# Kernel optimization log

Hardware: AMD Instinct MI355X
Metric: run time of the kernel (lower is better)

Reference implementation:

```python
import jax, jax.numpy as jnp
import numpy as np

NUM_GRAPHS = 1024
IN_F = 256
HID = 512


def setup_inputs() -> dict:
    key = jax.random.key(0)
    ks = jax.random.split(key, 20)
    s_in = 1.0 / np.sqrt(IN_F)
    s_h = 1.0 / np.sqrt(HID)
    inp = {
        "x": jax.random.normal(ks[0], (200000, IN_F), dtype=jnp.float32),
        "batch": jnp.sort(jax.random.randint(ks[1], (200000,), 0, NUM_GRAPHS)),
        # transforms: Linear(in_features -> hidden)
        "W_mean": jax.random.uniform(ks[2], (IN_F, HID), jnp.float32, -s_in, s_in),
        "b_mean": jax.random.uniform(ks[3], (HID,), jnp.float32, -s_in, s_in),
        "W_max": jax.random.uniform(ks[4], (IN_F, HID), jnp.float32, -s_in, s_in),
        "b_max": jax.random.uniform(ks[5], (HID,), jnp.float32, -s_in, s_in),
        "W_sum": jax.random.uniform(ks[6], (IN_F, HID), jnp.float32, -s_in, s_in),
        "b_sum": jax.random.uniform(ks[7], (HID,), jnp.float32, -s_in, s_in),
        # gates: Linear(hidden -> 1) + sigmoid
        "g_mean_w": jax.random.uniform(ks[8], (HID, 1), jnp.float32, -s_h, s_h),
        "g_mean_b": jax.random.uniform(ks[9], (1,), jnp.float32, -s_h, s_h),
        "g_max_w": jax.random.uniform(ks[10], (HID, 1), jnp.float32, -s_h, s_h),
        "g_max_b": jax.random.uniform(ks[11], (1,), jnp.float32, -s_h, s_h),
        "g_sum_w": jax.random.uniform(ks[12], (HID, 1), jnp.float32, -s_h, s_h),
        "g_sum_b": jax.random.uniform(ks[13], (1,), jnp.float32, -s_h, s_h),
        # output proj: Linear(hidden -> in_features)
        "W_out": jax.random.uniform(ks[14], (HID, IN_F), jnp.float32, -s_h, s_h),
        "b_out": jax.random.uniform(ks[15], (IN_F,), jnp.float32, -s_h, s_h),
        # layer norm params
        "ln_gamma": jnp.ones((IN_F,), jnp.float32),
        "ln_beta": jnp.zeros((IN_F,), jnp.float32),
    }
    return inp


def reference(x, batch, W_mean, b_mean, W_max, b_max, W_sum, b_sum,
              g_mean_w, g_mean_b, g_max_w, g_max_b, g_sum_w, g_sum_b,
              W_out, b_out, ln_gamma, ln_beta):
    # --- segment pools over node dim ---
    sum_pool = jax.ops.segment_sum(x, batch, num_segments=NUM_GRAPHS)  # [G, F]
    counts = jax.ops.segment_sum(jnp.ones((x.shape[0],), x.dtype), batch,
                                 num_segments=NUM_GRAPHS)  # [G]
    mean_pool = sum_pool / jnp.maximum(counts, 1.0)[:, None]
    max_pool = jax.ops.segment_max(x, batch, num_segments=NUM_GRAPHS)
    max_pool = jnp.where(counts[:, None] > 0, max_pool, 0.0)

    # --- per-pool linear transforms ---
    mean_repr = mean_pool @ W_mean + b_mean  # [G, H]
    max_repr = max_pool @ W_max + b_max
    sum_repr = sum_pool @ W_sum + b_sum

    # --- gated fusion ---
    g_mean = jax.nn.sigmoid(mean_repr @ g_mean_w + g_mean_b)  # [G, 1]
    g_max = jax.nn.sigmoid(max_repr @ g_max_w + g_max_b)
    g_sum = jax.nn.sigmoid(sum_repr @ g_sum_w + g_sum_b)
    gates = jax.nn.softmax(jnp.concatenate([g_mean, g_max, g_sum], axis=1), axis=1)
    pooled = (gates[:, 0:1] * mean_repr + gates[:, 1:2] * max_repr
              + gates[:, 2:3] * sum_repr)

    # --- output projection (+dropout as eval identity) + layer norm ---
    emb = pooled @ W_out + b_out  # [G, F]
    mu = jnp.mean(emb, axis=-1, keepdims=True)
    var = jnp.var(emb, axis=-1, keepdims=True)
    emb = (emb - mu) * jax.lax.rsqrt(var + 1e-5) * ln_gamma + ln_beta
    return emb
```

## Files before the change

kernel.cpp:

```cpp
#include <hip/hip_runtime.h>
#include <math.h>

#define NUM_GRAPHS 1024
#define IN_F 256
#define HID 512

__device__ __forceinline__ int lower_bound_i(const int* __restrict__ b, int n, int v) {
    int lo = 0, hi = n;
    while (lo < hi) {
        int mid = (lo + hi) >> 1;
        if (b[mid] < v) lo = mid + 1; else hi = mid;
    }
    return lo;
}

__global__ __launch_bounds__(256) void pool_kernel(
    const float* __restrict__ x, const int* __restrict__ batch, int N,
    float* __restrict__ sum_pool, float* __restrict__ mean_pool,
    float* __restrict__ max_pool)
{
    int g = blockIdx.x;
    __shared__ int sb[2];
    if (threadIdx.x < 2) sb[threadIdx.x] = lower_bound_i(batch, N, g + (int)threadIdx.x);
    __syncthreads();
    int start = sb[0], end = sb[1];
    int f = threadIdx.x;
    const float* xp = x + f;
    float s = 0.f;
    float mx = -INFINITY;
    int r = start;
    for (; r + 8 <= end; r += 8) {
        float v0 = xp[(size_t)(r+0)*IN_F];
        float v1 = xp[(size_t)(r+1)*IN_F];
        float v2 = xp[(size_t)(r+2)*IN_F];
        float v3 = xp[(size_t)(r+3)*IN_F];
        float v4 = xp[(size_t)(r+4)*IN_F];
        float v5 = xp[(size_t)(r+5)*IN_F];
        float v6 = xp[(size_t)(r+6)*IN_F];
        float v7 = xp[(size_t)(r+7)*IN_F];
        s += ((v0+v1)+(v2+v3)) + ((v4+v5)+(v6+v7));
        mx = fmaxf(mx, fmaxf(fmaxf(fmaxf(v0,v1), fmaxf(v2,v3)),
                             fmaxf(fmaxf(v4,v5), fmaxf(v6,v7))));
    }
    for (; r < end; ++r) {
        float v = xp[(size_t)r*IN_F];
        s += v; mx = fmaxf(mx, v);
    }
    int cnt = end - start;
    float mean = s / fmaxf((float)cnt, 1.0f);
    if (cnt == 0) mx = 0.f;
    int o = g*IN_F + f;
    sum_pool[o]  = s;
    mean_pool[o] = mean;
    max_pool[o]  = mx;
}

#define BM 64
#define BN 32
#define BKK 32
__global__ __launch_bounds__(256) void transform_gemm(
    const float* __restrict__ p_mean, const float* __restrict__ p_max, const float* __restrict__ p_sum,
    const float* __restrict__ Wm, const float* __restrict__ bm_,
    const float* __restrict__ Wx, const float* __restrict__ bx_,
    const float* __restrict__ Wsm, const float* __restrict__ bs_,
    float* __restrict__ r_mean, float* __restrict__ r_max, float* __restrict__ r_sum)
{
    int z = blockIdx.z;
    const float* P    = (z==0) ? p_mean : (z==1) ? p_max : p_sum;
    const float* W    = (z==0) ? Wm     : (z==1) ? Wx    : Wsm;
    const float* bias = (z==0) ? bm_    : (z==1) ? bx_   : bs_;
    float* R          = (z==0) ? r_mean : (z==1) ? r_max : r_sum;

    __shared__ float As[BKK][BM+1];
    __shared__ float Bs[BKK][BN+1];
    int tid = threadIdx.x;
    int bm0 = blockIdx.y * BM;
    int bn0 = blockIdx.x * BN;
    int ty = tid >> 4, tx = tid & 15;
    int m0 = ty * 4, n0 = tx * 2;
    float acc[4][2] = {};

    for (int kc = 0; kc < IN_F; kc += BKK) {
        #pragma unroll
        for (int i = 0; i < 8; ++i) {
            int idx = tid + i*256;
            int rr = idx >> 5, cc = idx & 31;
            As[cc][rr] = P[(bm0 + rr)*IN_F + kc + cc];
        }
        #pragma unroll
        for (int i = 0; i < 4; ++i) {
            int idx = tid + i*256;
            int rr = idx >> 5, cc = idx & 31;
            Bs[rr][cc] = W[(kc + rr)*HID + bn0 + cc];
        }
        __syncthreads();
        #pragma unroll
        for (int k = 0; k < BKK; ++k) {
            float a0 = As[k][m0+0], a1 = As[k][m0+1];
            float a2 = As[k][m0+2], a3 = As[k][m0+3];
            float b0 = Bs[k][n0+0], b1 = Bs[k][n0+1];
            acc[0][0] += a0*b0; acc[0][1] += a0*b1;
            acc[1][0] += a1*b0; acc[1][1] += a1*b1;
            acc[2][0] += a2*b0; acc[2][1] += a2*b1;
            acc[3][0] += a3*b0; acc[3][1] += a3*b1;
        }
        __syncthreads();
    }
    #pragma unroll
    for (int i = 0; i < 4; ++i) {
        #pragma unroll
        for (int j = 0; j < 2; ++j) {
            int row = bm0 + m0 + i, col = bn0 + n0 + j;
            R[(size_t)row*HID + col] = acc[i][j] + bias[col];
        }
    }
}

__global__ __launch_bounds__(256) void gate_fuse(
    const float* __restrict__ r_mean, const float* __restrict__ r_max, const float* __restrict__ r_sum,
    const float* __restrict__ gwm, const float* __restrict__ gbm,
    const float* __restrict__ gwx, const float* __restrict__ gbx,
    const float* __restrict__ gws, const float* __restrict__ gbs,
    float* __restrict__ pooled)
{
    int g = blockIdx.x;
    int tid = threadIdx.x;
    size_t base = (size_t)g * HID;
    int h0 = tid, h1 = tid + 256;
    float m0 = r_mean[base+h0], m1 = r_mean[base+h1];
    float x0 = r_max[base+h0],  x1 = r_max[base+h1];
    float s0 = r_sum[base+h0],  s1 = r_sum[base+h1];
    float pm = m0*gwm[h0] + m1*gwm[h1];
    float px = x0*gwx[h0] + x1*gwx[h1];
    float ps = s0*gws[h0] + s1*gws[h1];
    #pragma unroll
    for (int off = 32; off > 0; off >>= 1) {
        pm += __shfl_xor(pm, off, 64);
        px += __shfl_xor(px, off, 64);
        ps += __shfl_xor(ps, off, 64);
    }
    __shared__ float red[3][4];
    __shared__ float wgt[3];
    int wv = tid >> 6, lane = tid & 63;
    if (lane == 0) { red[0][wv] = pm; red[1][wv] = px; red[2][wv] = ps; }
    __syncthreads();
    if (tid == 0) {
        float dm  = red[0][0]+red[0][1]+red[0][2]+red[0][3] + gbm[0];
        float dx  = red[1][0]+red[1][1]+red[1][2]+red[1][3] + gbx[0];
        float dsv = red[2][0]+red[2][1]+red[2][2]+red[2][3] + gbs[0];
        float sm = 1.f/(1.f+expf(-dm));
        float sx = 1.f/(1.f+expf(-dx));
        float ss = 1.f/(1.f+expf(-dsv));
        float em = expf(sm), ex = expf(sx), es = expf(ss);
        float inv = 1.f/(em+ex+es);
        wgt[0] = em*inv; wgt[1] = ex*inv; wgt[2] = es*inv;
    }
    __syncthreads();
    float wm = wgt[0], wxx = wgt[1], wss = wgt[2];
    pooled[base+h0] = wm*m0 + wxx*x0 + wss*s0;
    pooled[base+h1] = wm*m1 + wxx*x1 + wss*s1;
}

#define EM 4
__global__ __launch_bounds__(256) void outproj_ln(
    const float* __restrict__ pooled, const float* __restrict__ Wout, const float* __restrict__ bout,
    const float* __restrict__ gamma, const float* __restrict__ beta, float* __restrict__ out)
{
    int gbase = blockIdx.x * EM;
    int tid = threadIdx.x;
    __shared__ float Ps[EM][HID];
    __shared__ float Es[EM][IN_F];
    const float4* pp = (const float4*)(pooled + (size_t)gbase * HID);
    float4* ps4 = (float4*)&Ps[0][0];
    ps4[tid]       = pp[tid];
    ps4[tid + 256] = pp[tid + 256];
    __syncthreads();
    float acc0=0.f, acc1=0.f, acc2=0.f, acc3=0.f;
    int f = tid;
    #pragma unroll 4
    for (int k = 0; k < HID; ++k) {
        float w = Wout[(size_t)k*IN_F + f];
        acc0 += Ps[0][k]*w;
        acc1 += Ps[1][k]*w;
        acc2 += Ps[2][k]*w;
        acc3 += Ps[3][k]*w;
    }
    float bo = bout[f];
    Es[0][f] = acc0+bo; Es[1][f] = acc1+bo; Es[2][f] = acc2+bo; Es[3][f] = acc3+bo;
    __syncthreads();
    int w = tid >> 6;
    int lane = tid & 63;
    float v0 = Es[w][lane], v1 = Es[w][lane+64], v2 = Es[w][lane+128], v3 = Es[w][lane+192];
    float s  = v0+v1+v2+v3;
    float sq = v0*v0+v1*v1+v2*v2+v3*v3;
    #pragma unroll
    for (int off = 32; off > 0; off >>= 1) {
        s  += __shfl_xor(s, off, 64);
        sq += __shfl_xor(sq, off, 64);
    }
    float mu  = s * (1.0f/IN_F);
    float var = sq * (1.0f/IN_F) - mu*mu;
    float rs  = rsqrtf(var + 1e-5f);
    float* orow = out + (size_t)(gbase + w) * IN_F;
    orow[lane]     = (v0-mu)*rs*gamma[lane]     + beta[lane];
    orow[lane+64]  = (v1-mu)*rs*gamma[lane+64]  + beta[lane+64];
    orow[lane+128] = (v2-mu)*rs*gamma[lane+128] + beta[lane+128];
    orow[lane+192] = (v3-mu)*rs*gamma[lane+192] + beta[lane+192];
}

extern "C" void kernel_launch(void* const* d_in, const int* in_sizes, int n_in,
                              void* d_out, int out_size, void* d_ws, size_t ws_size,
                              hipStream_t stream)
{
    const float* x        = (const float*)d_in[0];
    const int*   batch    = (const int*)d_in[1];
    const float* W_mean   = (const float*)d_in[2];
    const float* b_mean   = (const float*)d_in[3];
    const float* W_max    = (const float*)d_in[4];
    const float* b_max    = (const float*)d_in[5];
    const float* W_sum    = (const float*)d_in[6];
    const float* b_sum    = (const float*)d_in[7];
    const float* g_mean_w = (const float*)d_in[8];
    const float* g_mean_b = (const float*)d_in[9];
    const float* g_max_w  = (const float*)d_in[10];
    const float* g_max_b  = (const float*)d_in[11];
    const float* g_sum_w  = (const float*)d_in[12];
    const float* g_sum_b  = (const float*)d_in[13];
    const float* W_out    = (const float*)d_in[14];
    const float* b_out    = (const float*)d_in[15];
    const float* ln_gamma = (const float*)d_in[16];
    const float* ln_beta  = (const float*)d_in[17];
    float* out = (float*)d_out;
    int N = in_sizes[1];

    float* ws        = (float*)d_ws;
    float* sum_pool  = ws;
    float* mean_pool = ws + (size_t)NUM_GRAPHS*IN_F;
    float* max_pool  = ws + (size_t)2*NUM_GRAPHS*IN_F;
    float* r_mean    = ws + (size_t)3*NUM_GRAPHS*IN_F;
    float* r_max     = r_mean + (size_t)NUM_GRAPHS*HID;
    float* r_sum     = r_max  + (size_t)NUM_GRAPHS*HID;
    float* pooled    = r_sum  + (size_t)NUM_GRAPHS*HID;

    pool_kernel<<<NUM_GRAPHS, 256, 0, stream>>>(x, batch, N, sum_pool, mean_pool, max_pool);

    dim3 gridC(HID/BN, NUM_GRAPHS/BM, 3);
    transform_gemm<<<gridC, 256, 0, stream>>>(mean_pool, max_pool, sum_pool,
                                              W_mean, b_mean, W_max, b_max, W_sum, b_sum,
                                              r_mean, r_max, r_sum);

    gate_fuse<<<NUM_GRAPHS, 256, 0, stream>>>(r_mean, r_max, r_sum,
                                              g_mean_w, g_mean_b, g_max_w, g_max_b,
                                              g_sum_w, g_sum_b, pooled);

    outproj_ln<<<NUM_GRAPHS/EM, 256, 0, stream>>>(pooled, W_out, b_out, ln_gamma, ln_beta, out);
}
```

Baseline: 409.3 us.

## Vectorize pooling, retile transform GEMM, fuse gating into output projection

The pooling kernel now has each wave handle interleaved rows with float4 loads and combines partial sums and maxes through shared memory. This increases load width and memory parallelism on the dominant streaming read of x. The transform GEMM moves to 64x64 tiles with 4x4 register microtiles and vectorized loads and stores. The gate kernel is merged into the output-projection and layernorm kernel, removing the pooled intermediate and one launch, at the cost of more shared memory per block.

```diff
diff --git a/kernel.cpp b/kernel.cpp
--- a/kernel.cpp
+++ b/kernel.cpp
@@ -24,40 +24,58 @@
     if (threadIdx.x < 2) sb[threadIdx.x] = lower_bound_i(batch, N, g + (int)threadIdx.x);
     __syncthreads();
     int start = sb[0], end = sb[1];
-    int f = threadIdx.x;
-    const float* xp = x + f;
-    float s = 0.f;
-    float mx = -INFINITY;
-    int r = start;
-    for (; r + 8 <= end; r += 8) {
-        float v0 = xp[(size_t)(r+0)*IN_F];
-        float v1 = xp[(size_t)(r+1)*IN_F];
-        float v2 = xp[(size_t)(r+2)*IN_F];
-        float v3 = xp[(size_t)(r+3)*IN_F];
-        float v4 = xp[(size_t)(r+4)*IN_F];
-        float v5 = xp[(size_t)(r+5)*IN_F];
-        float v6 = xp[(size_t)(r+6)*IN_F];
-        float v7 = xp[(size_t)(r+7)*IN_F];
-        s += ((v0+v1)+(v2+v3)) + ((v4+v5)+(v6+v7));
-        mx = fmaxf(mx, fmaxf(fmaxf(fmaxf(v0,v1), fmaxf(v2,v3)),
-                             fmaxf(fmaxf(v4,v5), fmaxf(v6,v7))));
-    }
-    for (; r < end; ++r) {
-        float v = xp[(size_t)r*IN_F];
-        s += v; mx = fmaxf(mx, v);
-    }
     int cnt = end - start;
-    float mean = s / fmaxf((float)cnt, 1.0f);
-    if (cnt == 0) mx = 0.f;
-    int o = g*IN_F + f;
-    sum_pool[o]  = s;
-    mean_pool[o] = mean;
-    max_pool[o]  = mx;
+    int w = threadIdx.x >> 6, lane = threadIdx.x & 63;
+    const float4* x4 = (const float4*)x;
+    float4 s = make_float4(0.f, 0.f, 0.f, 0.f);
+    float4 m = make_float4(-INFINITY, -INFINITY, -INFINITY, -INFINITY);
+    int r = start + w;
+    for (; r + 12 < end; r += 16) {
+        float4 v0 = x4[(size_t)(r     )*64 + lane];
+        float4 v1 = x4[(size_t)(r +  4)*64 + lane];
+        float4 v2 = x4[(size_t)(r +  8)*64 + lane];
+        float4 v3 = x4[(size_t)(r + 12)*64 + lane];
+        s.x += (v0.x+v1.x)+(v2.x+v3.x); s.y += (v0.y+v1.y)+(v2.y+v3.y);
+        s.z += (v0.z+v1.z)+(v2.z+v3.z); s.w += (v0.w+v1.w)+(v2.w+v3.w);
+        m.x = fmaxf(m.x, fmaxf(fmaxf(v0.x,v1.x), fmaxf(v2.x,v3.x)));
+        m.y = fmaxf(m.y, fmaxf(fmaxf(v0.y,v1.y), fmaxf(v2.y,v3.y)));
+        m.z = fmaxf(m.z, fmaxf(fmaxf(v0.z,v1.z), fmaxf(v2.z,v3.z)));
+        m.w = fmaxf(m.w, fmaxf(fmaxf(v0.w,v1.w), fmaxf(v2.w,v3.w)));
+    }
+    for (; r < end; r += 4) {
+        float4 v = x4[(size_t)r*64 + lane];
+        s.x += v.x; s.y += v.y; s.z += v.z; s.w += v.w;
+        m.x = fmaxf(m.x, v.x); m.y = fmaxf(m.y, v.y);
+        m.z = fmaxf(m.z, v.z); m.w = fmaxf(m.w, v.w);
+    }
+    __shared__ float4 Ls[4][64];
+    __shared__ float4 Lm[4][64];
+    Ls[w][lane] = s; Lm[w][lane] = m;
+    __syncthreads();
+    if (w == 0) {
+        float4 s0 = Ls[0][lane], s1 = Ls[1][lane], s2 = Ls[2][lane], s3 = Ls[3][lane];
+        float4 m0 = Lm[0][lane], m1 = Lm[1][lane], m2 = Lm[2][lane], m3 = Lm[3][lane];
+        float4 st, mt;
+        st.x = (s0.x+s1.x)+(s2.x+s3.x); st.y = (s0.y+s1.y)+(s2.y+s3.y);
+        st.z = (s0.z+s1.z)+(s2.z+s3.z); st.w = (s0.w+s1.w)+(s2.w+s3.w);
+        mt.x = fmaxf(fmaxf(m0.x,m1.x), fmaxf(m2.x,m3.x));
+        mt.y = fmaxf(fmaxf(m0.y,m1.y), fmaxf(m2.y,m3.y));
+        mt.z = fmaxf(fmaxf(m0.z,m1.z), fmaxf(m2.z,m3.z));
+        mt.w = fmaxf(fmaxf(m0.w,m1.w), fmaxf(m2.w,m3.w));
+        float inv = 1.0f / fmaxf((float)cnt, 1.0f);
+        float4 me = make_float4(st.x*inv, st.y*inv, st.z*inv, st.w*inv);
+        if (cnt == 0) mt = make_float4(0.f, 0.f, 0.f, 0.f);
+        size_t o = (size_t)g*64 + lane;
+        ((float4*)sum_pool)[o]  = st;
+        ((float4*)mean_pool)[o] = me;
+        ((float4*)max_pool)[o]  = mt;
+    }
 }
 
 #define BM 64
-#define BN 32
-#define BKK 32
+#define BN 64
+#define BK 16
+#define LDA 68
 __global__ __launch_bounds__(256) void transform_gemm(
     const float* __restrict__ p_mean, const float* __restrict__ p_max, const float* __restrict__ p_sum,
     const float* __restrict__ Wm, const float* __restrict__ bm_,
@@ -71,137 +89,136 @@
     const float* bias = (z==0) ? bm_    : (z==1) ? bx_   : bs_;
     float* R          = (z==0) ? r_mean : (z==1) ? r_max : r_sum;
 
-    __shared__ float As[BKK][BM+1];
-    __shared__ float Bs[BKK][BN+1];
+    __shared__ float As[BK][LDA];
+    __shared__ float Bs[BK][LDA];
     int tid = threadIdx.x;
     int bm0 = blockIdx.y * BM;
     int bn0 = blockIdx.x * BN;
-    int ty = tid >> 4, tx = tid & 15;
-    int m0 = ty * 4, n0 = tx * 2;
-    float acc[4][2] = {};
-
-    for (int kc = 0; kc < IN_F; kc += BKK) {
+    int tx = tid & 15, ty = tid >> 4;
+    int arow = tid >> 2, akq = (tid & 3) * 4;
+    int brow = tid >> 4, bn4 = (tid & 15) * 4;
+    float acc[4][4] = {};
+
+    for (int kc = 0; kc < IN_F; kc += BK) {
+        float4 av = *(const float4*)&P[(size_t)(bm0 + arow)*IN_F + kc + akq];
+        float4 bv = *(const float4*)&W[(size_t)(kc + brow)*HID + bn0 + bn4];
+        As[akq+0][arow] = av.x; As[akq+1][arow] = av.y;
+        As[akq+2][arow] = av.z; As[akq+3][arow] = av.w;
+        *(float4*)&Bs[brow][bn4] = bv;
+        __syncthreads();
         #pragma unroll
-        for (int i = 0; i < 8; ++i) {
-            int idx = tid + i*256;
-            int rr = idx >> 5, cc = idx & 31;
-            As[cc][rr] = P[(bm0 + rr)*IN_F + kc + cc];
-        }
-        #pragma unroll
-        for (int i = 0; i < 4; ++i) {
-            int idx = tid + i*256;
-            int rr = idx >> 5, cc = idx & 31;
-            Bs[rr][cc] = W[(kc + rr)*HID + bn0 + cc];
+        for (int k = 0; k < BK; ++k) {
+            float4 a = *(const float4*)&As[k][ty*4];
+            float4 b = *(const float4*)&Bs[k][tx*4];
+            acc[0][0] += a.x*b.x; acc[0][1] += a.x*b.y; acc[0][2] += a.x*b.z; acc[0][3] += a.x*b.w;
+            acc[1][0] += a.y*b.x; acc[1][1] += a.y*b.y; acc[1][2] += a.y*b.z; acc[1][3] += a.y*b.w;
+            acc[2][0] += a.z*b.x; acc[2][1] += a.z*b.y; acc[2][2] += a.z*b.z; acc[2][3] += a.z*b.w;
+            acc[3][0] += a.w*b.x; acc[3][1] += a.w*b.y; acc[3][2] += a.w*b.z; acc[3][3] += a.w*b.w;
         }
         __syncthreads();
-        #pragma unroll
-        for (int k = 0; k < BKK; ++k) {
-            float a0 = As[k][m0+0], a1 = As[k][m0+1];
-            float a2 = As[k][m0+2], a3 = As[k][m0+3];
-            float b0 = Bs[k][n0+0], b1 = Bs[k][n0+1];
-            acc[0][0] += a0*b0; acc[0][1] += a0*b1;
-            acc[1][0] += a1*b0; acc[1][1] += a1*b1;
-            acc[2][0] += a2*b0; acc[2][1] += a2*b1;
-            acc[3][0] += a3*b0; acc[3][1] += a3*b1;
-        }
-        __syncthreads();
-    }
+    }
+    float4 b4 = *(const float4*)&bias[bn0 + tx*4];
     #pragma unroll
     for (int i = 0; i < 4; ++i) {
-        #pragma unroll
-        for (int j = 0; j < 2; ++j) {
-            int row = bm0 + m0 + i, col = bn0 + n0 + j;
-            R[(size_t)row*HID + col] = acc[i][j] + bias[col];
-        }
-    }
-}
-
-__global__ __launch_bounds__(256) void gate_fuse(
+        float4 o = make_float4(acc[i][0]+b4.x, acc[i][1]+b4.y, acc[i][2]+b4.z, acc[i][3]+b4.w);
+        *(float4*)&R[(size_t)(bm0 + ty*4 + i)*HID + bn0 + tx*4] = o;
+    }
+}
+
+#define EM 4
+__global__ __launch_bounds__(256) void gate_outproj_ln(
     const float* __restrict__ r_mean, const float* __restrict__ r_max, const float* __restrict__ r_sum,
     const float* __restrict__ gwm, const float* __restrict__ gbm,
     const float* __restrict__ gwx, const float* __restrict__ gbx,
     const float* __restrict__ gws, const float* __restrict__ gbs,
-    float* __restrict__ pooled)
-{
-    int g = blockIdx.x;
+    const float* __restrict__ Wout, const float* __restrict__ bout,
+    const float* __restrict__ gamma, const float* __restrict__ beta,
+    float* __restrict__ out)
+{
+    int g0 = blockIdx.x * EM;
     int tid = threadIdx.x;
-    size_t base = (size_t)g * HID;
-    int h0 = tid, h1 = tid + 256;
-    float m0 = r_mean[base+h0], m1 = r_mean[base+h1];
-    float x0 = r_max[base+h0],  x1 = r_max[base+h1];
-    float s0 = r_sum[base+h0],  s1 = r_sum[base+h1];
-    float pm = m0*gwm[h0] + m1*gwm[h1];
-    float px = x0*gwx[h0] + x1*gwx[h1];
-    float ps = s0*gws[h0] + s1*gws[h1];
-    #pragma unroll
-    for (int off = 32; off > 0; off >>= 1) {
-        pm += __shfl_xor(pm, off, 64);
-        px += __shfl_xor(px, off, 64);
-        ps += __shfl_xor(ps, off, 64);
-    }
-    __shared__ float red[3][4];
-    __shared__ float wgt[3];
-    int wv = tid >> 6, lane = tid & 63;
-    if (lane == 0) { red[0][wv] = pm; red[1][wv] = px; red[2][wv] = ps; }
-    __syncthreads();
-    if (tid == 0) {
-        float dm  = red[0][0]+red[0][1]+red[0][2]+red[0][3] + gbm[0];
-        float dx  = red[1][0]+red[1][1]+red[1][2]+red[1][3] + gbx[0];
-        float dsv = red[2][0]+red[2][1]+red[2][2]+red[2][3] + gbs[0];
-        float sm = 1.f/(1.f+expf(-dm));
-        float sx = 1.f/(1.f+expf(-dx));
-        float ss = 1.f/(1.f+expf(-dsv));
-        float em = expf(sm), ex = expf(sx), es = expf(ss);
-        float inv = 1.f/(em+ex+es);
-        wgt[0] = em*inv; wgt[1] = ex*inv; wgt[2] = es*inv;
-    }
-    __syncthreads();
-    float wm = wgt[0], wxx = wgt[1], wss = wgt[2];
-    pooled[base+h0] = wm*m0 + wxx*x0 + wss*s0;
-    pooled[base+h1] = wm*m1 + wxx*x1 + wss*s1;
-}
-
-#define EM 4
-__global__ __launch_bounds__(256) void outproj_ln(
-    const float* __restrict__ pooled, const float* __restrict__ Wout, const float* __restrict__ bout,
-    const float* __restrict__ gamma, const float* __restrict__ beta, float* __restrict__ out)
-{
-    int gbase = blockIdx.x * EM;
-    int tid = threadIdx.x;
+    __shared__ float Rm[EM][HID], Rx[EM][HID], Rs[EM][HID];
     __shared__ float Ps[EM][HID];
     __shared__ float Es[EM][IN_F];
-    const float4* pp = (const float4*)(pooled + (size_t)gbase * HID);
-    float4* ps4 = (float4*)&Ps[0][0];
-    ps4[tid]       = pp[tid];
-    ps4[tid + 256] = pp[tid + 256];
-    __syncthreads();
-    float acc0=0.f, acc1=0.f, acc2=0.f, acc3=0.f;
+    __shared__ float wgt[EM][3];
+
+    const float4* rm4 = (const float4*)(r_mean + (size_t)g0*HID);
+    const float4* rx4 = (const float4*)(r_max  + (size_t)g0*HID);
+    const float4* rs4 = (const float4*)(r_sum  + (size_t)g0*HID);
+    #pragma unroll
+    for (int i = 0; i < 2; ++i) {
+        int idx = tid + i*256;
+        ((float4*)Rm)[idx] = rm4[idx];
+        ((float4*)Rx)[idx] = rx4[idx];
+        ((float4*)Rs)[idx] = rs4[idx];
+    }
+    __syncthreads();
+
+    int w = tid >> 6, lane = tid & 63;
+    float dm = 0.f, dx = 0.f, dsv = 0.f;
+    #pragma unroll
+    for (int j = 0; j < 8; ++j) {
+        int k = lane + j*64;
+        dm  += Rm[w][k] * gwm[k];
+        dx  += Rx[w][k] * gwx[k];
+        dsv += Rs[w][k] * gws[k];
+    }
+    #pragma unroll
+    for (int off = 32; off > 0; off >>= 1) {
+        dm  += __shfl_xor(dm,  off, 64);
+        dx  += __shfl_xor(dx,  off, 64);
+        dsv += __shfl_xor(dsv, off, 64);
+    }
+    if (lane == 0) {
+        float sm = 1.f/(1.f + expf(-(dm  + gbm[0])));
+        float sx = 1.f/(1.f + expf(-(dx  + gbx[0])));
+        float ss = 1.f/(1.f + expf(-(dsv + gbs[0])));
+        float em = expf(sm), ex = expf(sx), es = expf(ss);
+        float inv = 1.f/(em + ex + es);
+        wgt[w][0] = em*inv; wgt[w][1] = ex*inv; wgt[w][2] = es*inv;
+    }
+    __syncthreads();
+
+    #pragma unroll
+    for (int i = 0; i < 8; ++i) {
+        int e = tid + i*256;
+        int j = e >> 9, k = e & 511;
+        Ps[j][k] = wgt[j][0]*Rm[j][k] + wgt[j][1]*Rx[j][k] + wgt[j][2]*Rs[j][k];
+    }
+    __syncthreads();
+
+    float a0 = 0.f, a1 = 0.f, a2 = 0.f, a3 = 0.f;
     int f = tid;
-    #pragma unroll 4
-    for (int k = 0; k < HID; ++k) {
-        float w = Wout[(size_t)k*IN_F + f];
-        acc0 += Ps[0][k]*w;
-        acc1 += Ps[1][k]*w;
-        acc2 += Ps[2][k]*w;
-        acc3 += Ps[3][k]*w;
+    for (int k = 0; k < HID; k += 4) {
+        float4 p0 = *(const float4*)&Ps[0][k];
+        float4 p1 = *(const float4*)&Ps[1][k];
+        float4 p2 = *(const float4*)&Ps[2][k];
+        float4 p3 = *(const float4*)&Ps[3][k];
+        float w0 = Wout[(size_t)(k+0)*IN_F + f];
+        float w1 = Wout[(size_t)(k+1)*IN_F + f];
+        float w2 = Wout[(size_t)(k+2)*IN_F + f];
+        float w3 = Wout[(size_t)(k+3)*IN_F + f];
+        a0 += p0.x*w0 + p0.y*w1 + p0.z*w2 + p0.w*w3;
+        a1 += p1.x*w0 + p1.y*w1 + p1.z*w2 + p1.w*w3;
+        a2 += p2.x*w0 + p2.y*w1 + p2.z*w2 + p2.w*w3;
+        a3 += p3.x*w0 + p3.y*w1 + p3.z*w2 + p3.w*w3;
     }
     float bo = bout[f];
-    Es[0][f] = acc0+bo; Es[1][f] = acc1+bo; Es[2][f] = acc2+bo; Es[3][f] = acc3+bo;
-    __syncthreads();
-    int w = tid >> 6;
-    int lane = tid & 63;
+    Es[0][f] = a0 + bo; Es[1][f] = a1 + bo; Es[2][f] = a2 + bo; Es[3][f] = a3 + bo;
+    __syncthreads();
+
     float v0 = Es[w][lane], v1 = Es[w][lane+64], v2 = Es[w][lane+128], v3 = Es[w][lane+192];
-    float s  = v0+v1+v2+v3;
-    float sq = v0*v0+v1*v1+v2*v2+v3*v3;
+    float s  = (v0+v1) + (v2+v3);
+    float sq = (v0*v0 + v1*v1) + (v2*v2 + v3*v3);
     #pragma unroll
     for (int off = 32; off > 0; off >>= 1) {
-        s  += __shfl_xor(s, off, 64);
+        s  += __shfl_xor(s,  off, 64);
         sq += __shfl_xor(sq, off, 64);
     }
     float mu  = s * (1.0f/IN_F);
     float var = sq * (1.0f/IN_F) - mu*mu;
     float rs  = rsqrtf(var + 1e-5f);
-    float* orow = out + (size_t)(gbase + w) * IN_F;
+    float* orow = out + (size_t)(g0 + w)*IN_F;
     orow[lane]     = (v0-mu)*rs*gamma[lane]     + beta[lane];
     orow[lane+64]  = (v1-mu)*rs*gamma[lane+64]  + beta[lane+64];
     orow[lane+128] = (v2-mu)*rs*gamma[lane+128] + beta[lane+128];
@@ -240,7 +257,6 @@
     float* r_mean    = ws + (size_t)3*NUM_GRAPHS*IN_F;
     float* r_max     = r_mean + (size_t)NUM_GRAPHS*HID;
     float* r_sum     = r_max  + (size_t)NUM_GRAPHS*HID;
-    float* pooled    = r_sum  + (size_t)NUM_GRAPHS*HID;
 
     pool_kernel<<<NUM_GRAPHS, 256, 0, stream>>>(x, batch, N, sum_pool, mean_pool, max_pool);
 
@@ -249,9 +265,8 @@
                                               W_mean, b_mean, W_max, b_max, W_sum, b_sum,
                                               r_mean, r_max, r_sum);
 
-    gate_fuse<<<NUM_GRAPHS, 256, 0, stream>>>(r_mean, r_max, r_sum,
-                                              g_mean_w, g_mean_b, g_max_w, g_max_b,
-                                              g_sum_w, g_sum_b, pooled);
-
-    outproj_ln<<<NUM_GRAPHS/EM, 256, 0, stream>>>(pooled, W_out, b_out, ln_gamma, ln_beta, out);
-}
+    gate_outproj_ln<<<NUM_GRAPHS/EM, 256, 0, stream>>>(r_mean, r_max, r_sum,
+                                                       g_mean_w, g_mean_b, g_max_w, g_max_b,
+                                                       g_sum_w, g_sum_b,
+                                                       W_out, b_out, ln_gamma, ln_beta, out);
+}
```

Measured after the change: 404.5 us. No clear change (-1.2%).
